# Performance work log

Measured on AMD Instinct MI355X. Metric: run time of the kernel, lower is better.

The kernel has to match this reference:

```python
import jax, jax.numpy as jnp
import numpy as np

NU, NI, D, E = 100000, 50000, 128, 500000


def setup_inputs() -> dict:
    key = jax.random.key(0)
    ks = jax.random.split(key, 10)
    s = 1.0 / np.sqrt(D)
    return {
        "feat_user": jax.random.normal(ks[0], (NU, D), jnp.float32),
        "feat_item": jax.random.normal(ks[1], (NI, D), jnp.float32),
        "W1": jax.random.normal(ks[2], (D, D), jnp.float32) * s,
        "b1": jnp.zeros((D,), jnp.float32),
        "W2": jax.random.normal(ks[3], (D, D), jnp.float32) * s,
        "b2": jnp.zeros((D,), jnp.float32),
        "norm_u2i": jax.random.uniform(ks[4], (E, 1), jnp.float32),
        "norm_i2u": jax.random.uniform(ks[5], (E, 1), jnp.float32),
        "edge_u2i_src": jax.random.randint(ks[6], (E,), 0, NU, jnp.int32),
        "edge_u2i_dst": jax.random.randint(ks[7], (E,), 0, NI, jnp.int32),
        "edge_i2u_src": jax.random.randint(ks[8], (E,), 0, NI, jnp.int32),
        "edge_i2u_dst": jax.random.randint(ks[9], (E,), 0, NU, jnp.int32),
    }


def reference(feat_user, feat_item, W1, b1, W2, b2, norm_u2i, norm_i2u,
              edge_u2i_src, edge_u2i_dst, edge_i2u_src, edge_i2u_dst):
    lin1 = lambda x: x @ W1 + b1
    lin2 = lambda x: x @ W2 + b2

    # self-loop etypes: copy_u(W1(feat)) summed over one self-edge per node
    h_user = lin1(feat_user)
    h_item = lin1(feat_item)

    # user -> item edges: norm * (W1(e_u) + W2(e_u * e_i)), scatter-sum to items
    su = feat_user[edge_u2i_src]            # [E, D]
    di = feat_item[edge_u2i_dst]            # [E, D]
    m_ui = norm_u2i * (lin1(su) + lin2(su * di))
    h_item = h_item + jax.ops.segment_sum(m_ui, edge_u2i_dst, num_segments=feat_item.shape[0])

    # item -> user edges
    si = feat_item[edge_i2u_src]
    du = feat_user[edge_i2u_dst]
    m_iu = norm_i2u * (lin1(si) + lin2(si * du))
    h_user = h_user + jax.ops.segment_sum(m_iu, edge_i2u_dst, num_segments=feat_user.shape[0])

    def finish(h):
        h = jax.nn.leaky_relu(h, 0.2)       # LeakyReLU(0.2); dropout p=0 is identity
        n = jnp.linalg.norm(h, axis=1, keepdims=True)
        return h / jnp.maximum(n, 1e-12)    # F.normalize(dim=1, p=2), eps=1e-12

    return finish(h_user), finish(h_item)
```

## Files before the change

kernel.cpp:

```cpp
#include <hip/hip_runtime.h>

#define DD 128
#define SCAN_TILE 1024

typedef __attribute__((ext_vector_type(8))) short short8;
typedef __attribute__((ext_vector_type(4))) float f32x4;

__device__ inline unsigned short f2bf_rne(float f) {
    unsigned int u = __float_as_uint(f);
    unsigned int r = u + 0x7FFFu + ((u >> 16) & 1u);
    return (unsigned short)(r >> 16);
}
__device__ inline float bf2f(unsigned short h) {
    return __uint_as_float(((unsigned int)h) << 16);
}
__device__ inline void split2(float a, float b, unsigned int& hi, unsigned int& lo) {
    unsigned short ha = f2bf_rne(a), hb = f2bf_rne(b);
    float la = a - bf2f(ha), lb = b - bf2f(hb);
    hi = (unsigned int)ha | ((unsigned int)hb << 16);
    lo = (unsigned int)f2bf_rne(la) | ((unsigned int)f2bf_rne(lb) << 16);
}


__global__ __launch_bounds__(256) void count_kernel(
    const int* __restrict__ dst1, int E1, int* deg1,
    const int* __restrict__ dst2, int E2, int* deg2)
{
    int t = blockIdx.x * 256 + threadIdx.x;
    if (t < E1) {
        atomicAdd(deg1 + dst1[t], 1);
    } else if (t - E1 < E2) {
        atomicAdd(deg2 + dst2[t - E1], 1);
    }
}

__global__ __launch_bounds__(256) void scanA_kernel(
    const int* __restrict__ cur_i, int NI,
    const int* __restrict__ cur_u, int NU,
    int* bsum, int nb0)
{
    int b = blockIdx.x;
    const int* cur;
    int N, base;
    if (b < nb0) { cur = cur_i; N = NI; base = b * SCAN_TILE; }
    else         { cur = cur_u; N = NU; base = (b - nb0) * SCAN_TILE; }
    int t = threadIdx.x;
    int idx0 = base + t * 4;
    int s = 0;
    #pragma unroll
    for (int k = 0; k < 4; ++k) {
        int idx = idx0 + k;
        if (idx < N) s += cur[idx];
    }
    __shared__ int red[256];
    red[t] = s;
    __syncthreads();
    for (int o = 128; o >= 1; o >>= 1) {
        if (t < o) red[t] += red[t + o];
        __syncthreads();
    }
    if (t == 0) bsum[b] = red[0];
}

__device__ int block_exscan_inplace(int* a, int n)
{
    __shared__ int sh[256];
    int t = threadIdx.x;
    int carry = 0;
    for (int base = 0; base < n; base += 256) {
        int v = (base + t < n) ? a[base + t] : 0;
        sh[t] = v;
        __syncthreads();
        for (int off = 1; off < 256; off <<= 1) {
            int u = (t >= off) ? sh[t - off] : 0;
            __syncthreads();
            sh[t] += u;
            __syncthreads();
        }
        if (base + t < n) a[base + t] = carry + sh[t] - v;
        int csum = sh[255];
        __syncthreads();
        carry += csum;
    }
    return carry;
}

__global__ __launch_bounds__(256) void scanB_kernel(
    int* bsum, int nb0, int nb1,
    int* row_i, int NI, int* row_u, int NU)
{
    int tot0 = block_exscan_inplace(bsum, nb0);
    __syncthreads();
    int tot1 = block_exscan_inplace(bsum + nb0, nb1);
    if (threadIdx.x == 0) {
        row_i[NI] = tot0;
        row_u[NU] = tot1;
    }
}

__global__ __launch_bounds__(256) void scanC_kernel(
    int* cur_i, int* row_i, int NI,
    int* cur_u, int* row_u, int NU,
    const int* __restrict__ bsum, int nb0)
{
    int b = blockIdx.x;
    int off = bsum[b];
    int* cur; int* row;
    int N, base;
    if (b < nb0) { cur = cur_i; row = row_i; N = NI; base = b * SCAN_TILE; }
    else         { cur = cur_u; row = row_u; N = NU; base = (b - nb0) * SCAN_TILE; }
    int t = threadIdx.x;
    int idx0 = base + t * 4;
    int v[4];
    int s = 0;
    #pragma unroll
    for (int k = 0; k < 4; ++k) {
        int idx = idx0 + k;
        v[k] = (idx < N) ? cur[idx] : 0;
        s += v[k];
    }
    __shared__ int sh[256];
    sh[t] = s;
    __syncthreads();
    for (int o = 1; o < 256; o <<= 1) {
        int u = (t >= o) ? sh[t - o] : 0;
        __syncthreads();
        sh[t] += u;
        __syncthreads();
    }
    int run = off + sh[t] - s;
    #pragma unroll
    for (int k = 0; k < 4; ++k) {
        int idx = idx0 + k;
        if (idx < N) {
            row[idx] = run;
            cur[idx] = run;
            run += v[k];
        }
    }
}

__global__ __launch_bounds__(256) void fill_pg_kernel(
    const int* __restrict__ dst1, const int* __restrict__ src1,
    const float* __restrict__ norm1, int E1, int* cur1, int* ss1, float* ns1,
    const int* __restrict__ dst2, const int* __restrict__ src2,
    const float* __restrict__ norm2, int E2, int* cur2, int* ss2, float* ns2)
{
    int t = blockIdx.x * 256 + threadIdx.x;
    if (t < E1) {
        int pos = atomicAdd(cur1 + dst1[t], 1);
        ss1[pos] = src1[t];
        ns1[pos] = norm1[t];
    } else if (t - E1 < E2) {
        int e = t - E1;
        int pos = atomicAdd(cur2 + dst2[e], 1);
        ss2[pos] = src2[e];
        ns2[pos] = norm2[e];
    }
}

__global__ __launch_bounds__(256) void gather_kernel(
    const int* __restrict__ row_i, const int* __restrict__ srcs1,
    const float* __restrict__ norms1,
    const float* __restrict__ feat_user, float* agg_item, float* ssum_i, int NI,
    const int* __restrict__ row_u, const int* __restrict__ srcs2,
    const float* __restrict__ norms2,
    const float* __restrict__ feat_item, float* agg_user, float* ssum_u, int NU)
{
    int gw = (int)((blockIdx.x * 256u + threadIdx.x) >> 6);
    int lane = threadIdx.x & 63;
    if (gw >= NI + NU) return;

    const int *row, *srcs;
    const float *norms, *feat;
    float *agg, *ssum;
    int d;
    if (gw < NI) {
        d = gw;      row = row_i; srcs = srcs1; norms = norms1;
        feat = feat_user; agg = agg_item; ssum = ssum_i;
    } else {
        d = gw - NI; row = row_u; srcs = srcs2; norms = norms2;
        feat = feat_item; agg = agg_user; ssum = ssum_u;
    }

    int beg = row[d], end = row[d + 1];
    float2 acc = {0.f, 0.f};
    float sn = 0.f;
    int j = beg;
    for (; j + 4 <= end; j += 4) {
        int s0 = srcs[j], s1 = srcs[j + 1], s2 = srcs[j + 2], s3 = srcs[j + 3];
        float n0 = norms[j],     n1 = norms[j + 1];
        float n2 = norms[j + 2], n3 = norms[j + 3];
        float2 v0 = *(const float2*)(feat + (size_t)s0 * DD + lane * 2);
        float2 v1 = *(const float2*)(feat + (size_t)s1 * DD + lane * 2);
        float2 v2 = *(const float2*)(feat + (size_t)s2 * DD + lane * 2);
        float2 v3 = *(const float2*)(feat + (size_t)s3 * DD + lane * 2);
        acc.x += n0 * v0.x + n1 * v1.x + n2 * v2.x + n3 * v3.x;
        acc.y += n0 * v0.y + n1 * v1.y + n2 * v2.y + n3 * v3.y;
        sn += n0 + n1 + n2 + n3;
    }
    for (; j < end; ++j) {
        int s0 = srcs[j];
        float n0 = norms[j];
        float2 v0 = *(const float2*)(feat + (size_t)s0 * DD + lane * 2);
        acc.x += n0 * v0.x;
        acc.y += n0 * v0.y;
        sn += n0;
    }
    float* ap = agg + (size_t)d * DD + lane * 2;
    __builtin_nontemporal_store(acc.x, ap);
    __builtin_nontemporal_store(acc.y, ap + 1);
    if (lane == 0) ssum[d] = sn;
}


__global__ __launch_bounds__(256) void scatter_kernel(
    const float* __restrict__ feat_src,
    const int* __restrict__ src,
    const int* __restrict__ dst,
    const float* __restrict__ norm,
    float* agg,
    float* ssum,
    int E)
{
    int gw = (int)((blockIdx.x * 256u + threadIdx.x) >> 6);
    int lane = threadIdx.x & 63;
    if (gw >= E) return;
    int si = src[gw];
    int di = dst[gw];
    float nv = norm[gw];
    float2 v = *(const float2*)(feat_src + (size_t)si * DD + lane * 2);
    float* ap = agg + (size_t)di * DD + lane * 2;
    unsafeAtomicAdd(ap,     v.x * nv);
    unsafeAtomicAdd(ap + 1, v.y * nv);
    if (lane == 0) unsafeAtomicAdd(ssum + di, nv);
}

__global__ __launch_bounds__(256) void wprep_kernel(
    const float* __restrict__ W1, const float* __restrict__ W2,
    unsigned short* wfrag)
{
    int t = blockIdx.x * 256 + threadIdx.x;
    if (t >= 4096) return;
    int lane = t & 63;
    int cf   = (t >> 6) & 7;
    int ksm  = (t >> 9) & 3;
    int mat  = t >> 11;
    const float* W = mat ? W2 : W1;
    int g = lane >> 4, c = lane & 15;
    int n = cf * 16 + c;
    unsigned int hi[4], lo[4];
    #pragma unroll
    for (int p = 0; p < 4; ++p) {
        int k0 = ksm * 32 + g * 8 + p * 2;
        float v0 = W[(size_t)k0 * DD + n];
        float v1 = W[(size_t)(k0 + 1) * DD + n];
        split2(v0, v1, hi[p], lo[p]);
    }
    unsigned short* dh = wfrag + (size_t)mat * 32768
                       + ((size_t)(ksm * 8 + cf) * 64 + lane) * 8;
    unsigned short* dl = dh + 16384;
    *(uint4*)dh = make_uint4(hi[0], hi[1], hi[2], hi[3]);
    *(uint4*)dl = make_uint4(lo[0], lo[1], lo[2], lo[3]);
}

__global__ __launch_bounds__(256) void finish_mfma_kernel(
    const float* __restrict__ feat_u, const float* aggu,
    const float* __restrict__ ssum_u, int NU, int nbU,
    const float* __restrict__ feat_i, const float* aggi,
    const float* __restrict__ ssum_i, int NI,
    const unsigned short* __restrict__ wfrag,
    const float* __restrict__ b1, const float* __restrict__ b2,
    float* out_base)
{
    __shared__ __align__(16) unsigned short Ah[32 * 256];
    __shared__ __align__(16) unsigned short Al[32 * 256];
    __shared__ float sst[32];

    const float *feat, *agg, *ssum;
    float* out;
    int row0, nrows;
    if ((int)blockIdx.x < nbU) {
        feat = feat_u; agg = aggu; ssum = ssum_u;
        out = out_base; row0 = blockIdx.x * 32; nrows = NU;
    } else {
        feat = feat_i; agg = aggi; ssum = ssum_i;
        out = out_base + (size_t)NU * DD;
        row0 = (blockIdx.x - nbU) * 32; nrows = NI;
    }

    int t = threadIdx.x;

    {
        int r  = t >> 3;
        int kq = (t & 7) * 16;
        int grow = row0 + r;
        bool valid = grow < nrows;
        unsigned int XH[8], XL[8], YH[8], YL[8];
        #pragma unroll
        for (int q = 0; q < 4; ++q) {
            float4 f4 = {0.f, 0.f, 0.f, 0.f}, a4 = {0.f, 0.f, 0.f, 0.f};
            if (valid) {
                f4 = *(const float4*)(feat + (size_t)grow * DD + kq + q * 4);
                a4 = *(const float4*)(agg  + (size_t)grow * DD + kq + q * 4);
            }
            float x0 = f4.x + a4.x, x1 = f4.y + a4.y;
            float x2 = f4.z + a4.z, x3 = f4.w + a4.w;
            float y0 = f4.x * a4.x, y1 = f4.y * a4.y;
            float y2 = f4.z * a4.z, y3 = f4.w * a4.w;
            split2(x0, x1, XH[q * 2],     XL[q * 2]);
            split2(x2, x3, XH[q * 2 + 1], XL[q * 2 + 1]);
            split2(y0, y1, YH[q * 2],     YL[q * 2]);
            split2(y2, y3, YH[q * 2 + 1], YL[q * 2 + 1]);
        }
        int swz = (r & 7) << 4;
        char* pAh = (char*)Ah;
        char* pAl = (char*)Al;
        int rb = r * 512;
        int x0o = rb + ((kq * 2)            ^ swz);
        int x1o = rb + ((kq * 2 + 16)       ^ swz);
        int y0o = rb + ((256 + kq * 2)      ^ swz);
        int y1o = rb + ((256 + kq * 2 + 16) ^ swz);
        *(uint4*)(pAh + x0o) = make_uint4(XH[0], XH[1], XH[2], XH[3]);
        *(uint4*)(pAh + x1o) = make_uint4(XH[4], XH[5], XH[6], XH[7]);
        *(uint4*)(pAl + x0o) = make_uint4(XL[0], XL[1], XL[2], XL[3]);
        *(uint4*)(pAl + x1o) = make_uint4(XL[4], XL[5], XL[6], XL[7]);
        *(uint4*)(pAh + y0o) = make_uint4(YH[0], YH[1], YH[2], YH[3]);
        *(uint4*)(pAh + y1o) = make_uint4(YH[4], YH[5], YH[6], YH[7]);
        *(uint4*)(pAl + y0o) = make_uint4(YL[0], YL[1], YL[2], YL[3]);
        *(uint4*)(pAl + y1o) = make_uint4(YL[4], YL[5], YL[6], YL[7]);
        if (t < 32) sst[t] = (row0 + t < nrows) ? ssum[row0 + t] : 0.f;
    }
    __syncthreads();

    int lane = t & 63;
    int w = t >> 6;
    int r16 = lane & 15, g = lane >> 4;
    f32x4 acc00 = {0.f,0.f,0.f,0.f}, acc01 = {0.f,0.f,0.f,0.f};
    f32x4 acc10 = {0.f,0.f,0.f,0.f}, acc11 = {0.f,0.f,0.f,0.f};
    const char* cAh = (const char*)Ah;
    const char* cAl = (const char*)Al;
    int swzA = (r16 & 7) << 4;
    int ob0 = r16 * 512;
    int ob1 = (r16 + 16) * 512;

    #pragma unroll 2
    for (int ks = 0; ks < 8; ++ks) {
        int kb = ks * 64 + g * 16;
        int offx = kb ^ swzA;
        short8 a0h = *(const short8*)(cAh + ob0 + offx);
        short8 a0l = *(const short8*)(cAl + ob0 + offx);
        short8 a1h = *(const short8*)(cAh + ob1 + offx);
        short8 a1l = *(const short8*)(cAl + ob1 + offx);
        int mat = ks >> 2, ksm = ks & 3;
        const unsigned short* ph = wfrag + (size_t)mat * 32768;
        const unsigned short* pl = ph + 16384;
        int bo0 = ((ksm * 8 + w * 2) * 64 + lane) * 8;
        int bo1 = bo0 + 512;
        short8 b0h = *(const short8*)(ph + bo0);
        short8 b0l = *(const short8*)(pl + bo0);
        short8 b1h = *(const short8*)(ph + bo1);
        short8 b1l = *(const short8*)(pl + bo1);
        acc00 = __builtin_amdgcn_mfma_f32_16x16x32_bf16(a0h, b0h, acc00, 0, 0, 0);
        acc00 = __builtin_amdgcn_mfma_f32_16x16x32_bf16(a0h, b0l, acc00, 0, 0, 0);
        acc00 = __builtin_amdgcn_mfma_f32_16x16x32_bf16(a0l, b0h, acc00, 0, 0, 0);
        acc01 = __builtin_amdgcn_mfma_f32_16x16x32_bf16(a0h, b1h, acc01, 0, 0, 0);
        acc01 = __builtin_amdgcn_mfma_f32_16x16x32_bf16(a0h, b1l, acc01, 0, 0, 0);
        acc01 = __builtin_amdgcn_mfma_f32_16x16x32_bf16(a0l, b1h, acc01, 0, 0, 0);
        acc10 = __builtin_amdgcn_mfma_f32_16x16x32_bf16(a1h, b0h, acc10, 0, 0, 0);
        acc10 = __builtin_amdgcn_mfma_f32_16x16x32_bf16(a1h, b0l, acc10, 0, 0, 0);
        acc10 = __builtin_amdgcn_mfma_f32_16x16x32_bf16(a1l, b0h, acc10, 0, 0, 0);
        acc11 = __builtin_amdgcn_mfma_f32_16x16x32_bf16(a1h, b1h, acc11, 0, 0, 0);
        acc11 = __builtin_amdgcn_mfma_f32_16x16x32_bf16(a1h, b1l, acc11, 0, 0, 0);
        acc11 = __builtin_amdgcn_mfma_f32_16x16x32_bf16(a1l, b1h, acc11, 0, 0, 0);
    }
    __syncthreads();

    float* hbuf = (float*)Ah;
    #pragma unroll
    for (int j = 0; j < 4; ++j) {
        int rA = g * 4 + j;
        hbuf[rA * DD        + (w * 32 + r16)]      = acc00[j];
        hbuf[rA * DD        + (w * 32 + 16 + r16)] = acc01[j];
        hbuf[(16 + rA) * DD + (w * 32 + r16)]      = acc10[j];
        hbuf[(16 + rA) * DD + (w * 32 + 16 + r16)] = acc11[j];
    }
    __syncthreads();

    int c0 = t & 63, c1 = c0 + 64, rg = t >> 6;
    float b1c0 = b1[c0], b1c1 = b1[c1];
    float b2c0 = b2[c0], b2c1 = b2[c1];
    #pragma unroll
    for (int rr = 0; rr < 8; ++rr) {
        int lr = rg * 8 + rr;
        int row = row0 + lr;
        if (row < nrows) {
            float s = sst[lr];
            float h0 = hbuf[lr * DD + c0] + (1.0f + s) * b1c0 + s * b2c0;
            float h1 = hbuf[lr * DD + c1] + (1.0f + s) * b1c1 + s * b2c1;
            h0 = h0 >= 0.f ? h0 : 0.2f * h0;
            h1 = h1 >= 0.f ? h1 : 0.2f * h1;
            float loc = h0 * h0 + h1 * h1;
            #pragma unroll
            for (int m = 32; m >= 1; m >>= 1) loc += __shfl_xor(loc, m, 64);
            float inv = 1.0f / fmaxf(sqrtf(loc), 1e-12f);
            out[(size_t)row * DD + c0] = h0 * inv;
            out[(size_t)row * DD + c1] = h1 * inv;
        }
    }
}


__global__ __launch_bounds__(256) void finish_kernel(
    const float* __restrict__ feat,
    const float* agg,
    const float* __restrict__ ssum,
    const float* __restrict__ W1,
    const float* __restrict__ b1,
    const float* __restrict__ W2,
    const float* __restrict__ b2,
    float* out,
    int nrows)
{
    __shared__ float xs[32][DD];
    __shared__ float ys[32][DD];
    int row0 = blockIdx.x * 32;
    int tid = threadIdx.x;

    for (int i = tid; i < 32 * (DD / 4); i += 256) {
        int r = i >> 5;
        int c4 = (i & 31) * 4;
        int row = row0 + r;
        if (row < nrows) {
            float4 f = *(const float4*)(feat + (size_t)row * DD + c4);
            float4 a = *(const float4*)(agg  + (size_t)row * DD + c4);
            float4 x, y;
            x.x = f.x + a.x; x.y = f.y + a.y; x.z = f.z + a.z; x.w = f.w + a.w;
            y.x = f.x * a.x; y.y = f.y * a.y; y.z = f.z * a.z; y.w = f.w * a.w;
            *(float4*)&xs[r][c4] = x;
            *(float4*)&ys[r][c4] = y;
        }
    }
    __syncthreads();

    int c0 = tid & 63;
    int rg = tid >> 6;
    int c1 = c0 + 64;

    float acc[8][2] = {{0.f,0.f},{0.f,0.f},{0.f,0.f},{0.f,0.f},
                       {0.f,0.f},{0.f,0.f},{0.f,0.f},{0.f,0.f}};
    for (int k = 0; k < DD; k += 4) {
        float w1a[4], w1b[4], w2a[4], w2b[4];
        #pragma unroll
        for (int kk = 0; kk < 4; ++kk) {
            const float* wr1 = W1 + (size_t)(k + kk) * DD;
            const float* wr2 = W2 + (size_t)(k + kk) * DD;
            w1a[kk] = wr1[c0]; w1b[kk] = wr1[c1];
            w2a[kk] = wr2[c0]; w2b[kk] = wr2[c1];
        }
        #pragma unroll
        for (int r = 0; r < 8; ++r) {
            float4 xv = *(const float4*)&xs[rg * 8 + r][k];
            float4 yv = *(const float4*)&ys[rg * 8 + r][k];
            acc[r][0] += xv.x*w1a[0] + xv.y*w1a[1] + xv.z*w1a[2] + xv.w*w1a[3]
                       + yv.x*w2a[0] + yv.y*w2a[1] + yv.z*w2a[2] + yv.w*w2a[3];
            acc[r][1] += xv.x*w1b[0] + xv.y*w1b[1] + xv.z*w1b[2] + xv.w*w1b[3]
                       + yv.x*w2b[0] + yv.y*w2b[1] + yv.z*w2b[2] + yv.w*w2b[3];
        }
    }

    float b1c0 = b1[c0], b1c1 = b1[c1];
    float b2c0 = b2[c0], b2c1 = b2[c1];

    #pragma unroll
    for (int r = 0; r < 8; ++r) {
        int row = row0 + rg * 8 + r;
        if (row < nrows) {
            float s = ssum[row];
            float h0 = acc[r][0] + (1.0f + s) * b1c0 + s * b2c0;
            float h1 = acc[r][1] + (1.0f + s) * b1c1 + s * b2c1;
            h0 = h0 >= 0.f ? h0 : 0.2f * h0;
            h1 = h1 >= 0.f ? h1 : 0.2f * h1;
            float loc = h0 * h0 + h1 * h1;
            #pragma unroll
            for (int m = 32; m >= 1; m >>= 1) loc += __shfl_xor(loc, m, 64);
            float inv = 1.0f / fmaxf(sqrtf(loc), 1e-12f);
            out[(size_t)row * DD + c0] = h0 * inv;
            out[(size_t)row * DD + c1] = h1 * inv;
        }
    }
}

extern "C" void kernel_launch(void* const* d_in, const int* in_sizes, int n_in,
                              void* d_out, int out_size, void* d_ws, size_t ws_size,
                              hipStream_t stream) {
    const float* feat_user = (const float*)d_in[0];
    const float* feat_item = (const float*)d_in[1];
    const float* W1        = (const float*)d_in[2];
    const float* b1        = (const float*)d_in[3];
    const float* W2        = (const float*)d_in[4];
    const float* b2        = (const float*)d_in[5];
    const float* norm_u2i  = (const float*)d_in[6];
    const float* norm_i2u  = (const float*)d_in[7];
    const int* eus = (const int*)d_in[8];
    const int* eud = (const int*)d_in[9];
    const int* eis = (const int*)d_in[10];
    const int* eid = (const int*)d_in[11];

    int NU = in_sizes[0] / DD;
    int NI = in_sizes[1] / DD;
    int E1 = in_sizes[8];
    int E2 = in_sizes[10];
    float* out = (float*)d_out;

    float* agg_user = out;
    float* agg_item = out + (size_t)NU * DD;

    int nb0 = (NI + SCAN_TILE - 1) / SCAN_TILE;
    int nb1 = (NU + SCAN_TILE - 1) / SCAN_TILE;
    int nbU = (NU + 31) / 32;
    int nbI = (NI + 31) / 32;

    size_t wfrag_bytes = 131072;
    size_t need_pg   = wfrag_bytes +
                       ((size_t)3 * NU + 3 * NI + 2 * E1 + 2 * E2 + 2
                        + nb0 + nb1) * sizeof(int);
    size_t need_perm = ((size_t)3 * NU + 3 * NI + E1 + E2 + 2
                        + nb0 + nb1) * sizeof(int);

    int eb = (int)(((long long)E1 + E2 + 255) / 256);
    int gb = (int)(((long long)(NI + NU) * 64 + 255) / 256);

    if (ws_size >= need_pg) {
        unsigned short* wfrag = (unsigned short*)d_ws;
        int* cur_i = (int*)((char*)d_ws + wfrag_bytes);
        int* cur_u = cur_i + NI;
        int* row_i = cur_u + NU;
        int* row_u = row_i + NI + 1;
        int* ss1   = row_u + NU + 1;
        int* ss2   = ss1 + E1;
        float* ns1 = (float*)(ss2 + E2);
        float* ns2 = ns1 + E1;
        float* ssum_i = ns2 + E2;
        float* ssum_u = ssum_i + NI;
        int* bsum = (int*)(ssum_u + NU);

        wprep_kernel<<<16, 256, 0, stream>>>(W1, W2, wfrag);

        hipMemsetAsync(cur_i, 0, (size_t)(NI + NU) * sizeof(int), stream);

        count_kernel<<<eb, 256, 0, stream>>>(eud, E1, cur_i, eid, E2, cur_u);
        scanA_kernel<<<nb0 + nb1, 256, 0, stream>>>(cur_i, NI, cur_u, NU,
                                                    bsum, nb0);
        scanB_kernel<<<1, 256, 0, stream>>>(bsum, nb0, nb1,
                                            row_i, NI, row_u, NU);
        scanC_kernel<<<nb0 + nb1, 256, 0, stream>>>(cur_i, row_i, NI,
                                                    cur_u, row_u, NU,
                                                    bsum, nb0);
        fill_pg_kernel<<<eb, 256, 0, stream>>>(
            eud, eus, norm_u2i, E1, cur_i, ss1, ns1,
            eid, eis, norm_i2u, E2, cur_u, ss2, ns2);

        gather_kernel<<<gb, 256, 0, stream>>>(
            row_i, ss1, ns1, feat_user, agg_item, ssum_i, NI,
            row_u, ss2, ns2, feat_item, agg_user, ssum_u, NU);

        finish_mfma_kernel<<<nbU + nbI, 256, 0, stream>>>(
            feat_user, agg_user, ssum_u, NU, nbU,
            feat_item, agg_item, ssum_i, NI,
            wfrag, b1, b2, out);
    } else if (ws_size >= need_perm) {
        int* cur_i = (int*)d_ws;
        int* cur_u = cur_i + NI;
        int* row_i = cur_u + NU;
        int* row_u = row_i + NI + 1;
        int* ss1   = row_u + NU + 1;
        int* ss2   = ss1 + E1;
        float* ssum_i = (float*)(ss2 + E2);
        float* ssum_u = ssum_i + NI;
        int* bsum = (int*)(ssum_u + NU);

        hipMemsetAsync(d_ws, 0, (size_t)(NI + NU) * sizeof(int), stream);

        count_kernel<<<eb, 256, 0, stream>>>(eud, E1, cur_i, eid, E2, cur_u);
        scanA_kernel<<<nb0 + nb1, 256, 0, stream>>>(cur_i, NI, cur_u, NU,
                                                    bsum, nb0);
        scanB_kernel<<<1, 256, 0, stream>>>(bsum, nb0, nb1,
                                            row_i, NI, row_u, NU);
        scanC_kernel<<<nb0 + nb1, 256, 0, stream>>>(cur_i, row_i, NI,
                                                    cur_u, row_u, NU,
                                                    bsum, nb0);
        hipMemsetAsync(out, 0, (size_t)out_size * sizeof(float), stream);
        hipMemsetAsync(ssum_i, 0, (size_t)(NI + NU) * sizeof(float), stream);
        int b1n = (int)(((long long)E1 * 64 + 255) / 256);
        scatter_kernel<<<b1n, 256, 0, stream>>>(feat_user, eus, eud, norm_u2i,
                                                agg_item, ssum_i, E1);
        int b2n = (int)(((long long)E2 * 64 + 255) / 256);
        scatter_kernel<<<b2n, 256, 0, stream>>>(feat_item, eis, eid, norm_i2u,
                                                agg_user, ssum_u, E2);
        finish_kernel<<<nbU, 256, 0, stream>>>(
            feat_user, agg_user, ssum_u, W1, b1, W2, b2, out, NU);
        finish_kernel<<<nbI, 256, 0, stream>>>(
            feat_item, agg_item, ssum_i, W1, b1, W2, b2,
            out + (size_t)NU * DD, NI);
    } else {
        float* s_user = (float*)d_ws;
        float* s_item = s_user + NU;

        hipMemsetAsync(out, 0, (size_t)out_size * sizeof(float), stream);
        hipMemsetAsync(d_ws, 0, (size_t)(NU + NI) * sizeof(float), stream);

        int b1n = (int)(((long long)E1 * 64 + 255) / 256);
        scatter_kernel<<<b1n, 256, 0, stream>>>(feat_user, eus, eud, norm_u2i,
                                                agg_item, s_item, E1);
        int b2n = (int)(((long long)E2 * 64 + 255) / 256);
        scatter_kernel<<<b2n, 256, 0, stream>>>(feat_item, eis, eid, norm_i2u,
                                                agg_user, s_user, E2);

        finish_kernel<<<nbU, 256, 0, stream>>>(
            feat_user, agg_user, s_user, W1, b1, W2, b2, out, NU);
        finish_kernel<<<nbI, 256, 0, stream>>>(
            feat_item, agg_item, s_item, W1, b1, W2, b2,
            out + (size_t)NU * DD, NI);
    }
}
```

Baseline: 420.2 us.

## Fuse CSR gather into MFMA finish kernel, pad hbuf stride, nontemporal output stores

Measured after the change: 418.6 us. No clear change (-0.4%).

```diff
diff --git a/kernel.cpp b/kernel.cpp
--- a/kernel.cpp
+++ b/kernel.cpp
@@ -2,6 +2,7 @@
 
 #define DD 128
 #define SCAN_TILE 1024
+#define HS 132
 
 typedef __attribute__((ext_vector_type(8))) short short8;
 typedef __attribute__((ext_vector_type(4))) float f32x4;
@@ -159,60 +160,6 @@
     }
 }
 
-__global__ __launch_bounds__(256) void gather_kernel(
-    const int* __restrict__ row_i, const int* __restrict__ srcs1,
-    const float* __restrict__ norms1,
-    const float* __restrict__ feat_user, float* agg_item, float* ssum_i, int NI,
-    const int* __restrict__ row_u, const int* __restrict__ srcs2,
-    const float* __restrict__ norms2,
-    const float* __restrict__ feat_item, float* agg_user, float* ssum_u, int NU)
-{
-    int gw = (int)((blockIdx.x * 256u + threadIdx.x) >> 6);
-    int lane = threadIdx.x & 63;
-    if (gw >= NI + NU) return;
-
-    const int *row, *srcs;
-    const float *norms, *feat;
-    float *agg, *ssum;
-    int d;
-    if (gw < NI) {
-        d = gw;      row = row_i; srcs = srcs1; norms = norms1;
-        feat = feat_user; agg = agg_item; ssum = ssum_i;
-    } else {
-        d = gw - NI; row = row_u; srcs = srcs2; norms = norms2;
-        feat = feat_item; agg = agg_user; ssum = ssum_u;
-    }
-
-    int beg = row[d], end = row[d + 1];
-    float2 acc = {0.f, 0.f};
-    float sn = 0.f;
-    int j = beg;
-    for (; j + 4 <= end; j += 4) {
-        int s0 = srcs[j], s1 = srcs[j + 1], s2 = srcs[j + 2], s3 = srcs[j + 3];
-        float n0 = norms[j],     n1 = norms[j + 1];
-        float n2 = norms[j + 2], n3 = norms[j + 3];
-        float2 v0 = *(const float2*)(feat + (size_t)s0 * DD + lane * 2);
-        float2 v1 = *(const float2*)(feat + (size_t)s1 * DD + lane * 2);
-        float2 v2 = *(const float2*)(feat + (size_t)s2 * DD + lane * 2);
-        float2 v3 = *(const float2*)(feat + (size_t)s3 * DD + lane * 2);
-        acc.x += n0 * v0.x + n1 * v1.x + n2 * v2.x + n3 * v3.x;
-        acc.y += n0 * v0.y + n1 * v1.y + n2 * v2.y + n3 * v3.y;
-        sn += n0 + n1 + n2 + n3;
-    }
-    for (; j < end; ++j) {
-        int s0 = srcs[j];
-        float n0 = norms[j];
-        float2 v0 = *(const float2*)(feat + (size_t)s0 * DD + lane * 2);
-        acc.x += n0 * v0.x;
-        acc.y += n0 * v0.y;
-        sn += n0;
-    }
-    float* ap = agg + (size_t)d * DD + lane * 2;
-    __builtin_nontemporal_store(acc.x, ap);
-    __builtin_nontemporal_store(acc.y, ap + 1);
-    if (lane == 0) ssum[d] = sn;
-}
-
 
 __global__ __launch_bounds__(256) void scatter_kernel(
     const float* __restrict__ feat_src,
@@ -264,11 +211,12 @@
     *(uint4*)dl = make_uint4(lo[0], lo[1], lo[2], lo[3]);
 }
 
-__global__ __launch_bounds__(256) void finish_mfma_kernel(
-    const float* __restrict__ feat_u, const float* aggu,
-    const float* __restrict__ ssum_u, int NU, int nbU,
-    const float* __restrict__ feat_i, const float* aggi,
-    const float* __restrict__ ssum_i, int NI,
+__global__ __launch_bounds__(256) void fused_kernel(
+    const float* __restrict__ feat_user, const float* __restrict__ feat_item,
+    const int* __restrict__ row_u, const int* __restrict__ ss2,
+    const float* __restrict__ ns2, int NU, int nbU,
+    const int* __restrict__ row_i, const int* __restrict__ ss1,
+    const float* __restrict__ ns1, int NI,
     const unsigned short* __restrict__ wfrag,
     const float* __restrict__ b1, const float* __restrict__ b2,
     float* out_base)
@@ -277,64 +225,73 @@
     __shared__ __align__(16) unsigned short Al[32 * 256];
     __shared__ float sst[32];
 
-    const float *feat, *agg, *ssum;
+    const float *featO, *featS, *ns;
+    const int *row, *ss;
     float* out;
     int row0, nrows;
     if ((int)blockIdx.x < nbU) {
-        feat = feat_u; agg = aggu; ssum = ssum_u;
+        featO = feat_user; featS = feat_item; row = row_u; ss = ss2; ns = ns2;
         out = out_base; row0 = blockIdx.x * 32; nrows = NU;
     } else {
-        feat = feat_i; agg = aggi; ssum = ssum_i;
+        featO = feat_item; featS = feat_user; row = row_i; ss = ss1; ns = ns1;
         out = out_base + (size_t)NU * DD;
         row0 = (blockIdx.x - nbU) * 32; nrows = NI;
     }
 
     int t = threadIdx.x;
-
-    {
-        int r  = t >> 3;
-        int kq = (t & 7) * 16;
+    int w = t >> 6;
+    int lane = t & 63;
+    char* pAh = (char*)Ah;
+    char* pAl = (char*)Al;
+
+    for (int rr = 0; rr < 8; ++rr) {
+        int r = w * 8 + rr;
         int grow = row0 + r;
-        bool valid = grow < nrows;
-        unsigned int XH[8], XL[8], YH[8], YL[8];
-        #pragma unroll
-        for (int q = 0; q < 4; ++q) {
-            float4 f4 = {0.f, 0.f, 0.f, 0.f}, a4 = {0.f, 0.f, 0.f, 0.f};
-            if (valid) {
-                f4 = *(const float4*)(feat + (size_t)grow * DD + kq + q * 4);
-                a4 = *(const float4*)(agg  + (size_t)grow * DD + kq + q * 4);
+        float2 acc = {0.f, 0.f};
+        float sn = 0.f;
+        float2 f2 = {0.f, 0.f};
+        if (grow < nrows) {
+            f2 = *(const float2*)(featO + (size_t)grow * DD + lane * 2);
+            int beg = row[grow], end = row[grow + 1];
+            int j = beg;
+            for (; j + 4 <= end; j += 4) {
+                int s0 = ss[j], s1 = ss[j + 1], s2 = ss[j + 2], s3 = ss[j + 3];
+                float n0 = ns[j],     n1 = ns[j + 1];
+                float n2 = ns[j + 2], n3 = ns[j + 3];
+                float2 v0 = *(const float2*)(featS + (size_t)s0 * DD + lane * 2);
+                float2 v1 = *(const float2*)(featS + (size_t)s1 * DD + lane * 2);
+                float2 v2 = *(const float2*)(featS + (size_t)s2 * DD + lane * 2);
+                float2 v3 = *(const float2*)(featS + (size_t)s3 * DD + lane * 2);
+                acc.x += n0 * v0.x + n1 * v1.x + n2 * v2.x + n3 * v3.x;
+                acc.y += n0 * v0.y + n1 * v1.y + n2 * v2.y + n3 * v3.y;
+                sn += n0 + n1 + n2 + n3;
             }
-            float x0 = f4.x + a4.x, x1 = f4.y + a4.y;
-            float x2 = f4.z + a4.z, x3 = f4.w + a4.w;
-            float y0 = f4.x * a4.x, y1 = f4.y * a4.y;
-            float y2 = f4.z * a4.z, y3 = f4.w * a4.w;
-            split2(x0, x1, XH[q * 2],     XL[q * 2]);
-            split2(x2, x3, XH[q * 2 + 1], XL[q * 2 + 1]);
-            split2(y0, y1, YH[q * 2],     YL[q * 2]);
-            split2(y2, y3, YH[q * 2 + 1], YL[q * 2 + 1]);
-        }
+            for (; j < end; ++j) {
+                int s0 = ss[j];
+                float n0 = ns[j];
+                float2 v0 = *(const float2*)(featS + (size_t)s0 * DD + lane * 2);
+                acc.x += n0 * v0.x;
+                acc.y += n0 * v0.y;
+                sn += n0;
+            }
+        }
+        float x0 = f2.x + acc.x, x1 = f2.y + acc.y;
+        float y0 = f2.x * acc.x, y1 = f2.y * acc.y;
+        unsigned int xh, xl, yh, yl;
+        split2(x0, x1, xh, xl);
+        split2(y0, y1, yh, yl);
         int swz = (r & 7) << 4;
-        char* pAh = (char*)Ah;
-        char* pAl = (char*)Al;
         int rb = r * 512;
-        int x0o = rb + ((kq * 2)            ^ swz);
-        int x1o = rb + ((kq * 2 + 16)       ^ swz);
-        int y0o = rb + ((256 + kq * 2)      ^ swz);
-        int y1o = rb + ((256 + kq * 2 + 16) ^ swz);
-        *(uint4*)(pAh + x0o) = make_uint4(XH[0], XH[1], XH[2], XH[3]);
-        *(uint4*)(pAh + x1o) = make_uint4(XH[4], XH[5], XH[6], XH[7]);
-        *(uint4*)(pAl + x0o) = make_uint4(XL[0], XL[1], XL[2], XL[3]);
-        *(uint4*)(pAl + x1o) = make_uint4(XL[4], XL[5], XL[6], XL[7]);
-        *(uint4*)(pAh + y0o) = make_uint4(YH[0], YH[1], YH[2], YH[3]);
-        *(uint4*)(pAh + y1o) = make_uint4(YH[4], YH[5], YH[6], YH[7]);
-        *(uint4*)(pAl + y0o) = make_uint4(YL[0], YL[1], YL[2], YL[3]);
-        *(uint4*)(pAl + y1o) = make_uint4(YL[4], YL[5], YL[6], YL[7]);
-        if (t < 32) sst[t] = (row0 + t < nrows) ? ssum[row0 + t] : 0.f;
-    }
-    __syncthreads();
-
-    int lane = t & 63;
-    int w = t >> 6;
+        int xo = rb + ((4 * lane) ^ swz);
+        int yo = rb + ((256 + 4 * lane) ^ swz);
+        *(unsigned int*)(pAh + xo) = xh;
+        *(unsigned int*)(pAl + xo) = xl;
+        *(unsigned int*)(pAh + yo) = yh;
+        *(unsigned int*)(pAl + yo) = yl;
+        if (lane == 0) sst[r] = sn;
+    }
+    __syncthreads();
+
     int r16 = lane & 15, g = lane >> 4;
     f32x4 acc00 = {0.f,0.f,0.f,0.f}, acc01 = {0.f,0.f,0.f,0.f};
     f32x4 acc10 = {0.f,0.f,0.f,0.f}, acc11 = {0.f,0.f,0.f,0.f};
@@ -380,10 +337,10 @@
     #pragma unroll
     for (int j = 0; j < 4; ++j) {
         int rA = g * 4 + j;
-        hbuf[rA * DD        + (w * 32 + r16)]      = acc00[j];
-        hbuf[rA * DD        + (w * 32 + 16 + r16)] = acc01[j];
-        hbuf[(16 + rA) * DD + (w * 32 + r16)]      = acc10[j];
-        hbuf[(16 + rA) * DD + (w * 32 + 16 + r16)] = acc11[j];
+        hbuf[rA * HS        + (w * 32 + r16)]      = acc00[j];
+        hbuf[rA * HS        + (w * 32 + 16 + r16)] = acc01[j];
+        hbuf[(16 + rA) * HS + (w * 32 + r16)]      = acc10[j];
+        hbuf[(16 + rA) * HS + (w * 32 + 16 + r16)] = acc11[j];
     }
     __syncthreads();
 
@@ -393,19 +350,19 @@
     #pragma unroll
     for (int rr = 0; rr < 8; ++rr) {
         int lr = rg * 8 + rr;
-        int row = row0 + lr;
-        if (row < nrows) {
+        int row_ = row0 + lr;
+        if (row_ < nrows) {
             float s = sst[lr];
-            float h0 = hbuf[lr * DD + c0] + (1.0f + s) * b1c0 + s * b2c0;
-            float h1 = hbuf[lr * DD + c1] + (1.0f + s) * b1c1 + s * b2c1;
+            float h0 = hbuf[lr * HS + c0] + (1.0f + s) * b1c0 + s * b2c0;
+            float h1 = hbuf[lr * HS + c1] + (1.0f + s) * b1c1 + s * b2c1;
             h0 = h0 >= 0.f ? h0 : 0.2f * h0;
             h1 = h1 >= 0.f ? h1 : 0.2f * h1;
             float loc = h0 * h0 + h1 * h1;
             #pragma unroll
             for (int m = 32; m >= 1; m >>= 1) loc += __shfl_xor(loc, m, 64);
             float inv = 1.0f / fmaxf(sqrtf(loc), 1e-12f);
-            out[(size_t)row * DD + c0] = h0 * inv;
-            out[(size_t)row * DD + c1] = h1 * inv;
+            __builtin_nontemporal_store(h0 * inv, out + (size_t)row_ * DD + c0);
+            __builtin_nontemporal_store(h1 * inv, out + (size_t)row_ * DD + c1);
         }
     }
 }
@@ -513,9 +470,6 @@
     int E2 = in_sizes[10];
     float* out = (float*)d_out;
 
-    float* agg_user = out;
-    float* agg_item = out + (size_t)NU * DD;
-
     int nb0 = (NI + SCAN_TILE - 1) / SCAN_TILE;
     int nb1 = (NU + SCAN_TILE - 1) / SCAN_TILE;
     int nbU = (NU + 31) / 32;
@@ -525,11 +479,8 @@
     size_t need_pg   = wfrag_bytes +
                        ((size_t)3 * NU + 3 * NI + 2 * E1 + 2 * E2 + 2
                         + nb0 + nb1) * sizeof(int);
-    size_t need_perm = ((size_t)3 * NU + 3 * NI + E1 + E2 + 2
-                        + nb0 + nb1) * sizeof(int);
 
     int eb = (int)(((long long)E1 + E2 + 255) / 256);
-    int gb = (int)(((long long)(NI + NU) * 64 + 255) / 256);
 
     if (ws_size >= need_pg) {
         unsigned short* wfrag = (unsigned short*)d_ws;
@@ -541,9 +492,7 @@
         int* ss2   = ss1 + E1;
         float* ns1 = (float*)(ss2 + E2);
         float* ns2 = ns1 + E1;
-        float* ssum_i = ns2 + E2;
-        float* ssum_u = ssum_i + NI;
-        int* bsum = (int*)(ssum_u + NU);
+        int* bsum  = (int*)(ns2 + E2);
 
         wprep_kernel<<<16, 256, 0, stream>>>(W1, W2, wfrag);
 
@@ -561,49 +510,14 @@
             eud, eus, norm_u2i, E1, cur_i, ss1, ns1,
             eid, eis, norm_i2u, E2, cur_u, ss2, ns2);
 
-        gather_kernel<<<gb, 256, 0, stream>>>(
-            row_i, ss1, ns1, feat_user, agg_item, ssum_i, NI,
-            row_u, ss2, ns2, feat_item, agg_user, ssum_u, NU);
-
-        finish_mfma_kernel<<<nbU + nbI, 256, 0, stream>>>(
-            feat_user, agg_user, ssum_u, NU, nbU,
-            feat_item, agg_item, ssum_i, NI,
+        fused_kernel<<<nbU + nbI, 256, 0, stream>>>(
+            feat_user, feat_item,
+            row_u, ss2, ns2, NU, nbU,
+            row_i, ss1, ns1, NI,
             wfrag, b1, b2, out);
-    } else if (ws_size >= need_perm) {
-        int* cur_i = (int*)d_ws;
-        int* cur_u = cur_i + NI;
-        int* row_i = cur_u + NU;
-        int* row_u = row_i + NI + 1;
-        int* ss1   = row_u + NU + 1;
-        int* ss2   = ss1 + E1;
-        float* ssum_i = (float*)(ss2 + E2);
-        float* ssum_u = ssum_i + NI;
-        int* bsum = (int*)(ssum_u + NU);
-
-        hipMemsetAsync(d_ws, 0, (size_t)(NI + NU) * sizeof(int), stream);
-
-        count_kernel<<<eb, 256, 0, stream>>>(eud, E1, cur_i, eid, E2, cur_u);
-        scanA_kernel<<<nb0 + nb1, 256, 0, stream>>>(cur_i, NI, cur_u, NU,
-                                                    bsum, nb0);
-        scanB_kernel<<<1, 256, 0, stream>>>(bsum, nb0, nb1,
-                                            row_i, NI, row_u, NU);
-        scanC_kernel<<<nb0 + nb1, 256, 0, stream>>>(cur_i, row_i, NI,
-                                                    cur_u, row_u, NU,
-                                                    bsum, nb0);
-        hipMemsetAsync(out, 0, (size_t)out_size * sizeof(float), stream);
-        hipMemsetAsync(ssum_i, 0, (size_t)(NI + NU) * sizeof(float), stream);
-        int b1n = (int)(((long long)E1 * 64 + 255) / 256);
-        scatter_kernel<<<b1n, 256, 0, stream>>>(feat_user, eus, eud, norm_u2i,
-                                                agg_item, ssum_i, E1);
-        int b2n = (int)(((long long)E2 * 64 + 255) / 256);
-        scatter_kernel<<<b2n, 256, 0, stream>>>(feat_item, eis, eid, norm_i2u,
-                                                agg_user, ssum_u, E2);
-        finish_kernel<<<nbU, 256, 0, stream>>>(
-            feat_user, agg_user, ssum_u, W1, b1, W2, b2, out, NU);
-        finish_kernel<<<nbI, 256, 0, stream>>>(
-            feat_item, agg_item, ssum_i, W1, b1, W2, b2,
-            out + (size_t)NU * DD, NI);
     } else {
+        float* agg_user = out;
+        float* agg_item = out + (size_t)NU * DD;
         float* s_user = (float*)d_ws;
         float* s_item = s_user + NU;
 
```
